# Optimization experiments

Hardware: AMD Instinct MI355X
Metric: run time of the kernel (lower is better)

Reference implementation:

```python
import jax, jax.numpy as jnp
import numpy as np

B, S, H, E, K = 4, 2048, 1024, 8, 2

def setup_inputs() -> dict:
    key = jax.random.key(0)
    k0, k1, k2, k3 = jax.random.split(key, 4)
    x = jax.random.normal(k0, (B, S, H), dtype=jnp.float32)
    # xavier-uniform-like scales
    router_w = jax.random.normal(k1, (E, H), dtype=jnp.float32) * np.float32(1.0 / np.sqrt(H))
    xav1 = np.float32(np.sqrt(2.0 / (2 * H + H)))
    w1 = jax.random.normal(k2, (E, 2 * H, H), dtype=jnp.float32) * xav1
    w2 = jax.random.normal(k3, (E, H, 2 * H), dtype=jnp.float32) * xav1
    return {"x": x, "router_w": router_w, "w1": w1, "w2": w2}

def reference(x, router_w, w1, w2):
    bsz, seq, hidden = x.shape
    n_experts = w1.shape[0]
    tokens = x.reshape(-1, hidden)                      # [T, H]
    T = tokens.shape[0]
    logits = tokens @ router_w.T                        # [T, E]
    topv, topi = jax.lax.top_k(logits, K)               # [T, K]
    w = jax.nn.softmax(topv, axis=-1).astype(tokens.dtype)
    # Dense gate matrix: gate[t, e] = routing weight of expert e for token t
    # (zero for non-selected experts). Equivalent to the torch pad/dispatch/
    # scatter-add combine: padded slots have weight 0 and contribute nothing.
    gate = jnp.zeros((T, n_experts), tokens.dtype).at[jnp.arange(T)[:, None], topi].add(w)
    out = jnp.zeros_like(tokens)
    for e in range(n_experts):  # small fixed expert count
        h = jax.nn.gelu(tokens @ w1[e].T, approximate=False)  # [T, 2H] (torch F.gelu = erf)
        y = h @ w2[e].T                                       # [T, H]
        out = out + gate[:, e:e + 1] * y
    return out.reshape(bsz, seq, hidden)
```

## Files before the change

### kernel.cpp

```cpp
#include <hip/hip_runtime.h>
#include <stdint.h>
#include <math.h>

#define T_TOK 8192
#define H_DIM 1024
#define H2    2048
#define NE    8

typedef unsigned short u16;
typedef __attribute__((ext_vector_type(8))) short bf16x8;
typedef __attribute__((ext_vector_type(4))) float f32x4;

__device__ __forceinline__ u16 f32_to_bf16(float f) {
  union { float f; unsigned u; } c; c.f = f;
  unsigned u = c.u + 0x7fffu + ((c.u >> 16) & 1u);
  return (u16)(u >> 16);
}
__device__ __forceinline__ float bf2f(u16 v) {
  union { unsigned u; float f; } c; c.u = (unsigned)v << 16; return c.f;
}

__device__ __forceinline__ float fast_gelu(float v) {
  float u = v * v;
  float z2 = v * fmaf(u, 0.1029437f, 2.3022078f);
  float e = __builtin_amdgcn_exp2f(z2);
  float r = __builtin_amdgcn_rcpf(1.0f + e);
  return v - v * r;
}

__device__ __forceinline__ void g2l16(const void* g, void* l) {
  __builtin_amdgcn_global_load_lds(
      (const __attribute__((address_space(1))) unsigned*)g,
      (__attribute__((address_space(3))) unsigned*)l, 16, 0, 0);
}

__device__ __forceinline__ int prefix_base(const int* counts, int e) {
  int b = 0;
#pragma unroll
  for (int j = 0; j < NE; j++) b += (j < e) ? counts[j] : 0;
  return b;
}

__global__ __launch_bounds__(256) void prep_kernel(
    const float* __restrict__ x, const float* __restrict__ rw,
    const float* __restrict__ w1, const float* __restrict__ w2,
    u16* __restrict__ xb, u16* __restrict__ w1b, u16* __restrict__ w2b,
    int* __restrict__ tope, float2* __restrict__ gate2,
    int* __restrict__ counts) {
  int blk = blockIdx.x;
  if (blk < T_TOK / 4) {
    int wave = threadIdx.x >> 6;
    int lane = threadIdx.x & 63;
    int t = blk * 4 + wave;
    const float4* x4 = (const float4*)(x + (size_t)t * H_DIM);
    const float4* rw4 = (const float4*)rw;
    u16* xbrow = xb + (size_t)t * H_DIM;

    double acc[NE];
#pragma unroll
    for (int e = 0; e < NE; e++) acc[e] = 0.0;
#pragma unroll
    for (int i = 0; i < 4; i++) {
      int c = lane + 64 * i;
      float4 xv = x4[c];
      ushort4 bv = make_ushort4(f32_to_bf16(xv.x), f32_to_bf16(xv.y),
                                f32_to_bf16(xv.z), f32_to_bf16(xv.w));
      *(ushort4*)(xbrow + c * 4) = bv;
#pragma unroll
      for (int e = 0; e < NE; e++) {
        float4 wv = rw4[e * 256 + c];
        acc[e] += (double)xv.x * wv.x + (double)xv.y * wv.y +
                  (double)xv.z * wv.z + (double)xv.w * wv.w;
      }
    }
#pragma unroll
    for (int off = 32; off >= 1; off >>= 1)
#pragma unroll
      for (int e = 0; e < NE; e++) acc[e] += __shfl_xor(acc[e], off, 64);

    if (lane == 0) {
      int e0 = 0; double v0 = acc[0];
#pragma unroll
      for (int e = 1; e < NE; e++) if (acc[e] > v0) { v0 = acc[e]; e0 = e; }
      int e1 = -1; double v1 = -1e300;
#pragma unroll
      for (int e = 0; e < NE; e++) if (e != e0 && acc[e] > v1) { v1 = acc[e]; e1 = e; }
      double ex = exp(v1 - v0);
      tope[t] = e0 | (e1 << 8);
      gate2[t] = make_float2((float)(1.0 / (1.0 + ex)), (float)(ex / (1.0 + ex)));
    }
  } else {
    int cb = blk - T_TOK / 4;
    if (cb == 0 && threadIdx.x < NE) counts[threadIdx.x] = 0;
    const float* src; u16* dst;
    if (cb < 3072) { src = w1; dst = w1b; }
    else           { src = w2; dst = w2b; cb -= 3072; }
    const int n4 = NE * H2 * H_DIM / 4;
    const int stride = 3072 * 256;
    const float4* s4 = (const float4*)src;
    for (int i = cb * 256 + threadIdx.x; i < n4; i += stride) {
      float4 v = s4[i];
      *(ushort4*)(dst + (size_t)i * 4) = make_ushort4(
          f32_to_bf16(v.x), f32_to_bf16(v.y), f32_to_bf16(v.z), f32_to_bf16(v.w));
    }
  }
}

__global__ __launch_bounds__(256) void build_kernel(
    const int* __restrict__ tope, int* __restrict__ counts,
    int* __restrict__ tok_list, int2* __restrict__ pos2) {
  __shared__ int cts[4][NE];
  __shared__ int gbase[NE];
  int tid = threadIdx.x, lane = tid & 63, w = tid >> 6;
  int t = blockIdx.x * 256 + tid;
  int pk = tope[t];
  int e0 = pk & 0xff, e1 = (pk >> 8) & 0xff;
  unsigned long long lt = ((unsigned long long)1 << lane) - 1;

  int r0 = 0, r1 = 0;
#pragma unroll
  for (int e = 0; e < NE; e++) {
    unsigned long long b0 = __ballot(e0 == e);
    unsigned long long b1 = __ballot(e1 == e);
    int n0 = __popcll(b0), n1 = __popcll(b1);
    if (e0 == e) r0 = __popcll(b0 & lt);
    if (e1 == e) r1 = n0 + __popcll(b1 & lt);
    if (lane == 0) cts[w][e] = n0 + n1;
  }
  __syncthreads();
  if (tid < NE) {
    int bt = cts[0][tid] + cts[1][tid] + cts[2][tid] + cts[3][tid];
    gbase[tid] = atomicAdd(&counts[tid], bt);
  }
  __syncthreads();
  int off0 = gbase[e0] + r0;
  int off1 = gbase[e1] + r1;
#pragma unroll
  for (int wp = 0; wp < 4; wp++) {
    if (wp < w) { off0 += cts[wp][e0]; off1 += cts[wp][e1]; }
  }
  tok_list[e0 * T_TOK + off0] = t;
  tok_list[e1 * T_TOK + off1] = t;
  pos2[t] = make_int2(off0, off1);
}

__global__ __launch_bounds__(256) void g1_kernel(
    const u16* __restrict__ xb, const u16* __restrict__ w1b,
    u16* __restrict__ h, const int* __restrict__ tok_list,
    const int* __restrict__ counts) {
  const int NT = H2 / 128;
  int e = blockIdx.x / (64 * NT);
  int rem = blockIdx.x % (64 * NT);
  int mt = rem / NT, nt = rem % NT;
  int cnt = counts[e];
  int m0 = mt * 128;
  if (m0 >= cnt) return;
  int base = prefix_base(counts, e);

  __shared__ u16 As[128 * 64];
  __shared__ u16 Bs[128 * 64];

  int tid = threadIdx.x;
  int lane = tid & 63, wave = tid >> 6;
  int wr = wave >> 1, wc = wave & 1;
  int quad = lane >> 4, l16 = lane & 15;
  int srow = tid >> 3;
  int cg = (tid & 7) ^ (srow & 7);

  const u16* w1e = w1b + (size_t)e * H2 * H_DIM;
  const u16* ap[4]; const u16* bp[4];
#pragma unroll
  for (int R = 0; R < 4; R++) {
    int r = m0 + R * 32 + srow; if (r > cnt - 1) r = cnt - 1;
    ap[R] = xb + (size_t)tok_list[e * T_TOK + r] * H_DIM + cg * 8;
    bp[R] = w1e + (size_t)(nt * 128 + R * 32 + srow) * H_DIM + cg * 8;
  }

  f32x4 acc[4][4];
#pragma unroll
  for (int i = 0; i < 4; i++)
#pragma unroll
    for (int j = 0; j < 4; j++)
#pragma unroll
      for (int r = 0; r < 4; r++) acc[i][j][r] = 0.f;

  int swz = l16 & 7;
  for (int k0 = 0; k0 < H_DIM; k0 += 64) {
#pragma unroll
    for (int R = 0; R < 4; R++) {
      g2l16(ap[R] + k0, As + R * 2048 + tid * 8);
      g2l16(bp[R] + k0, Bs + R * 2048 + tid * 8);
    }
    __syncthreads();
#pragma unroll
    for (int kk = 0; kk < 2; kk++) {
      bf16x8 af[4], bfr[4];
      int q = kk * 4 + quad;
#pragma unroll
      for (int mi = 0; mi < 4; mi++)
        af[mi] = *(const bf16x8*)(As + (wr * 64 + mi * 16 + l16) * 64 + ((q ^ swz) * 8));
#pragma unroll
      for (int ni = 0; ni < 4; ni++)
        bfr[ni] = *(const bf16x8*)(Bs + (wc * 64 + ni * 16 + l16) * 64 + ((q ^ swz) * 8));
#pragma unroll
      for (int mi = 0; mi < 4; mi++)
#pragma unroll
        for (int ni = 0; ni < 4; ni++)
          acc[mi][ni] = __builtin_amdgcn_mfma_f32_16x16x32_bf16(af[mi], bfr[ni], acc[mi][ni], 0, 0, 0);
    }
    __syncthreads();
  }

#pragma unroll
  for (int mi = 0; mi < 4; mi++) {
    int rbase = wr * 64 + mi * 16 + quad * 4;
#pragma unroll
    for (int r = 0; r < 4; r++) {
      int rr = m0 + rbase + r;
      if (rr < cnt) {
        size_t ho = (size_t)(base + rr) * H2 + nt * 128 + wc * 64 + l16;
#pragma unroll
        for (int ni = 0; ni < 4; ni++)
          h[ho + ni * 16] = f32_to_bf16(fast_gelu(acc[mi][ni][r]));
      }
    }
  }
}

__global__ __launch_bounds__(256) void g2_kernel(
    const u16* __restrict__ h, const u16* __restrict__ w2b,
    u16* __restrict__ y, const int* __restrict__ counts) {
  const int NT = H_DIM / 128;
  int e = blockIdx.x / (64 * NT);
  int rem = blockIdx.x % (64 * NT);
  int mt = rem / NT, nt = rem % NT;
  int cnt = counts[e];
  int m0 = mt * 128;
  if (m0 >= cnt) return;
  int base = prefix_base(counts, e);

  __shared__ u16 As[128 * 64];
  __shared__ u16 Bs[128 * 64];

  int tid = threadIdx.x;
  int lane = tid & 63, wave = tid >> 6;
  int wr = wave >> 1, wc = wave & 1;
  int quad = lane >> 4, l16 = lane & 15;
  int srow = tid >> 3;
  int cg = (tid & 7) ^ (srow & 7);

  const u16* w2e = w2b + (size_t)e * H_DIM * H2;
  const u16* ap[4]; const u16* bp[4];
#pragma unroll
  for (int R = 0; R < 4; R++) {
    int r = m0 + R * 32 + srow; if (r > cnt - 1) r = cnt - 1;
    ap[R] = h + (size_t)(base + r) * H2 + cg * 8;
    bp[R] = w2e + (size_t)(nt * 128 + R * 32 + srow) * H2 + cg * 8;
  }

  f32x4 acc[4][4];
#pragma unroll
  for (int i = 0; i < 4; i++)
#pragma unroll
    for (int j = 0; j < 4; j++)
#pragma unroll
      for (int r = 0; r < 4; r++) acc[i][j][r] = 0.f;

  int swz = l16 & 7;
  for (int k0 = 0; k0 < H2; k0 += 64) {
#pragma unroll
    for (int R = 0; R < 4; R++) {
      g2l16(ap[R] + k0, As + R * 2048 + tid * 8);
      g2l16(bp[R] + k0, Bs + R * 2048 + tid * 8);
    }
    __syncthreads();
#pragma unroll
    for (int kk = 0; kk < 2; kk++) {
      bf16x8 af[4], bfr[4];
      int q = kk * 4 + quad;
#pragma unroll
      for (int mi = 0; mi < 4; mi++)
        af[mi] = *(const bf16x8*)(As + (wr * 64 + mi * 16 + l16) * 64 + ((q ^ swz) * 8));
#pragma unroll
      for (int ni = 0; ni < 4; ni++)
        bfr[ni] = *(const bf16x8*)(Bs + (wc * 64 + ni * 16 + l16) * 64 + ((q ^ swz) * 8));
#pragma unroll
      for (int mi = 0; mi < 4; mi++)
#pragma unroll
        for (int ni = 0; ni < 4; ni++)
          acc[mi][ni] = __builtin_amdgcn_mfma_f32_16x16x32_bf16(af[mi], bfr[ni], acc[mi][ni], 0, 0, 0);
    }
    __syncthreads();
  }

#pragma unroll
  for (int mi = 0; mi < 4; mi++) {
    int rbase = wr * 64 + mi * 16 + quad * 4;
#pragma unroll
    for (int r = 0; r < 4; r++) {
      int rr = m0 + rbase + r;
      if (rr < cnt) {
        size_t yo = (size_t)(base + rr) * H_DIM + nt * 128 + wc * 64 + l16;
#pragma unroll
        for (int ni = 0; ni < 4; ni++)
          y[yo + ni * 16] = f32_to_bf16(acc[mi][ni][r]);
      }
    }
  }
}

__global__ __launch_bounds__(256) void combine_kernel(
    const u16* __restrict__ y, const int* __restrict__ tope,
    const float2* __restrict__ gate2, const int2* __restrict__ pos2,
    const int* __restrict__ counts, float* __restrict__ out) {
  int t = blockIdx.x;
  int pk = tope[t];
  int e0 = pk & 0xff, e1 = (pk >> 8) & 0xff;
  float2 g = gate2[t];
  int2 p = pos2[t];
  int hb0 = prefix_base(counts, e0);
  int hb1 = prefix_base(counts, e1);
  size_t s0 = (size_t)(hb0 + p.x) * H_DIM + threadIdx.x * 4;
  size_t s1 = (size_t)(hb1 + p.y) * H_DIM + threadIdx.x * 4;
  ushort4 a = *(const ushort4*)(y + s0);
  ushort4 b = *(const ushort4*)(y + s1);
  float4 o;
  o.x = g.x * bf2f(a.x) + g.y * bf2f(b.x);
  o.y = g.x * bf2f(a.y) + g.y * bf2f(b.y);
  o.z = g.x * bf2f(a.z) + g.y * bf2f(b.z);
  o.w = g.x * bf2f(a.w) + g.y * bf2f(b.w);
  *(float4*)(out + (size_t)t * H_DIM + threadIdx.x * 4) = o;
}

extern "C" void kernel_launch(void* const* d_in, const int* in_sizes, int n_in,
                              void* d_out, int out_size, void* d_ws, size_t ws_size,
                              hipStream_t stream) {
  const float* x  = (const float*)d_in[0];
  const float* rw = (const float*)d_in[1];
  const float* w1 = (const float*)d_in[2];
  const float* w2 = (const float*)d_in[3];
  float* out = (float*)d_out;

  char* ws = (char*)d_ws;
  u16* xb       = (u16*)(ws);
  u16* w1b      = (u16*)(ws + 16777216);
  u16* y        = (u16*)(ws + 16777216);
  u16* w2b      = (u16*)(ws + 50331648);
  u16* h        = (u16*)(ws + 83886080);
  int* tok_list = (int*)(ws + 150994944);
  int* tope     = (int*)(ws + 151257088);
  float2* gate2 = (float2*)(ws + 151289856);
  int2* pos2    = (int2*)(ws + 151355392);
  int* counts   = (int*)(ws + 151420928);

  prep_kernel<<<T_TOK / 4 + 6144, 256, 0, stream>>>(x, rw, w1, w2, xb, w1b, w2b,
                                                    tope, gate2, counts);
  build_kernel<<<T_TOK / 256, 256, 0, stream>>>(tope, counts, tok_list, pos2);
  g1_kernel<<<NE * 64 * (H2 / 128), 256, 0, stream>>>(xb, w1b, h, tok_list, counts);
  g2_kernel<<<NE * 64 * (H_DIM / 128), 256, 0, stream>>>(h, w2b, y, counts);
  combine_kernel<<<T_TOK, 256, 0, stream>>>(y, tope, gate2, pos2, counts, out);
}
```

Measured before the change: 406.8 us.

## Unify expert GEMMs into pipelined 256x256 tile kernel with 4-stage LDS ring

Replaces the two separate 128x128 expert GEMM kernels with one templated kernel that uses 256x256 output tiles, 512 threads (8 waves, 2x4), and a K-step of 32. Global-to-LDS loads go through a 4-deep buffer ring with explicit vmcnt waits, so loads for step k+3 are in flight while step k runs its MFMAs. The change also adds s_setprio around the MFMA block and drops the second barrier per iteration. The goal is to hide global memory latency and raise data reuse per tile. The cost is higher register pressure (128 accumulators per thread) and 128KB of LDS per block, and larger tiles waste more work on partial per-expert tiles.

New measurement: 400.8 us. Within noise of the previous version (-1.5%).

```diff
diff --git a/kernel.cpp b/kernel.cpp
--- a/kernel.cpp
+++ b/kernel.cpp
@@ -144,166 +144,112 @@
   pos2[t] = make_int2(off0, off1);
 }
 
-__global__ __launch_bounds__(256) void g1_kernel(
-    const u16* __restrict__ xb, const u16* __restrict__ w1b,
-    u16* __restrict__ h, const int* __restrict__ tok_list,
+template <int NK, int NT, int OUTN, bool GATHER, bool GELU>
+__global__ __launch_bounds__(512, 2) void moe_gemm(
+    const u16* __restrict__ A, const u16* __restrict__ W,
+    u16* __restrict__ O, const int* __restrict__ tok_list,
     const int* __restrict__ counts) {
-  const int NT = H2 / 128;
-  int e = blockIdx.x / (64 * NT);
-  int rem = blockIdx.x % (64 * NT);
+  const int MTMAX = T_TOK / 256;
+  int e = blockIdx.x / (MTMAX * NT);
+  int rem = blockIdx.x % (MTMAX * NT);
   int mt = rem / NT, nt = rem % NT;
   int cnt = counts[e];
-  int m0 = mt * 128;
+  int m0 = mt * 256;
   if (m0 >= cnt) return;
   int base = prefix_base(counts, e);
-
-  __shared__ u16 As[128 * 64];
-  __shared__ u16 Bs[128 * 64];
+  const int K = NK * 32;
+
+  __shared__ u16 lA[4][8192];
+  __shared__ u16 lB[4][8192];
 
   int tid = threadIdx.x;
   int lane = tid & 63, wave = tid >> 6;
-  int wr = wave >> 1, wc = wave & 1;
+  int wr = wave >> 2, wc = wave & 3;
   int quad = lane >> 4, l16 = lane & 15;
-  int srow = tid >> 3;
-  int cg = (tid & 7) ^ (srow & 7);
-
-  const u16* w1e = w1b + (size_t)e * H2 * H_DIM;
-  const u16* ap[4]; const u16* bp[4];
-#pragma unroll
-  for (int R = 0; R < 4; R++) {
-    int r = m0 + R * 32 + srow; if (r > cnt - 1) r = cnt - 1;
-    ap[R] = xb + (size_t)tok_list[e * T_TOK + r] * H_DIM + cg * 8;
-    bp[R] = w1e + (size_t)(nt * 128 + R * 32 + srow) * H_DIM + cg * 8;
-  }
-
-  f32x4 acc[4][4];
-#pragma unroll
-  for (int i = 0; i < 4; i++)
+
+  int cg = (tid & 3) ^ ((tid >> 3) & 3);
+  const u16* We = W + (size_t)e * OUTN * K;
+  const u16* asrc[2]; const u16* bsrc[2];
+#pragma unroll
+  for (int r = 0; r < 2; ++r) {
+    int row = (tid >> 2) + 128 * r;
+    int ar = m0 + row; if (ar > cnt - 1) ar = cnt - 1;
+    if (GATHER) asrc[r] = A + (size_t)tok_list[e * T_TOK + ar] * K + cg * 8;
+    else        asrc[r] = A + (size_t)(base + ar) * K + cg * 8;
+    bsrc[r] = We + (size_t)(nt * 256 + row) * K + cg * 8;
+  }
+
+  auto stage = [&](int kt) {
+    int b = kt & 3;
+#pragma unroll
+    for (int r = 0; r < 2; ++r) {
+      g2l16(asrc[r] + kt * 32, &lA[b][r * 4096 + tid * 8]);
+      g2l16(bsrc[r] + kt * 32, &lB[b][r * 4096 + tid * 8]);
+    }
+  };
+
+  f32x4 acc[8][4];
+#pragma unroll
+  for (int i = 0; i < 8; i++)
 #pragma unroll
     for (int j = 0; j < 4; j++)
 #pragma unroll
       for (int r = 0; r < 4; r++) acc[i][j][r] = 0.f;
 
-  int swz = l16 & 7;
-  for (int k0 = 0; k0 < H_DIM; k0 += 64) {
-#pragma unroll
-    for (int R = 0; R < 4; R++) {
-      g2l16(ap[R] + k0, As + R * 2048 + tid * 8);
-      g2l16(bp[R] + k0, Bs + R * 2048 + tid * 8);
-    }
-    __syncthreads();
-#pragma unroll
-    for (int kk = 0; kk < 2; kk++) {
-      bf16x8 af[4], bfr[4];
-      int q = kk * 4 + quad;
-#pragma unroll
-      for (int mi = 0; mi < 4; mi++)
-        af[mi] = *(const bf16x8*)(As + (wr * 64 + mi * 16 + l16) * 64 + ((q ^ swz) * 8));
-#pragma unroll
-      for (int ni = 0; ni < 4; ni++)
-        bfr[ni] = *(const bf16x8*)(Bs + (wc * 64 + ni * 16 + l16) * 64 + ((q ^ swz) * 8));
-#pragma unroll
-      for (int mi = 0; mi < 4; mi++)
-#pragma unroll
-        for (int ni = 0; ni < 4; ni++)
-          acc[mi][ni] = __builtin_amdgcn_mfma_f32_16x16x32_bf16(af[mi], bfr[ni], acc[mi][ni], 0, 0, 0);
-    }
-    __syncthreads();
-  }
-
-#pragma unroll
-  for (int mi = 0; mi < 4; mi++) {
-    int rbase = wr * 64 + mi * 16 + quad * 4;
-#pragma unroll
-    for (int r = 0; r < 4; r++) {
-      int rr = m0 + rbase + r;
-      if (rr < cnt) {
-        size_t ho = (size_t)(base + rr) * H2 + nt * 128 + wc * 64 + l16;
-#pragma unroll
-        for (int ni = 0; ni < 4; ni++)
-          h[ho + ni * 16] = f32_to_bf16(fast_gelu(acc[mi][ni][r]));
-      }
-    }
-  }
-}
-
-__global__ __launch_bounds__(256) void g2_kernel(
-    const u16* __restrict__ h, const u16* __restrict__ w2b,
-    u16* __restrict__ y, const int* __restrict__ counts) {
-  const int NT = H_DIM / 128;
-  int e = blockIdx.x / (64 * NT);
-  int rem = blockIdx.x % (64 * NT);
-  int mt = rem / NT, nt = rem % NT;
-  int cnt = counts[e];
-  int m0 = mt * 128;
-  if (m0 >= cnt) return;
-  int base = prefix_base(counts, e);
-
-  __shared__ u16 As[128 * 64];
-  __shared__ u16 Bs[128 * 64];
-
-  int tid = threadIdx.x;
-  int lane = tid & 63, wave = tid >> 6;
-  int wr = wave >> 1, wc = wave & 1;
-  int quad = lane >> 4, l16 = lane & 15;
-  int srow = tid >> 3;
-  int cg = (tid & 7) ^ (srow & 7);
-
-  const u16* w2e = w2b + (size_t)e * H_DIM * H2;
-  const u16* ap[4]; const u16* bp[4];
-#pragma unroll
-  for (int R = 0; R < 4; R++) {
-    int r = m0 + R * 32 + srow; if (r > cnt - 1) r = cnt - 1;
-    ap[R] = h + (size_t)(base + r) * H2 + cg * 8;
-    bp[R] = w2e + (size_t)(nt * 128 + R * 32 + srow) * H2 + cg * 8;
-  }
-
-  f32x4 acc[4][4];
-#pragma unroll
-  for (int i = 0; i < 4; i++)
-#pragma unroll
-    for (int j = 0; j < 4; j++)
-#pragma unroll
-      for (int r = 0; r < 4; r++) acc[i][j][r] = 0.f;
-
-  int swz = l16 & 7;
-  for (int k0 = 0; k0 < H2; k0 += 64) {
-#pragma unroll
-    for (int R = 0; R < 4; R++) {
-      g2l16(ap[R] + k0, As + R * 2048 + tid * 8);
-      g2l16(bp[R] + k0, Bs + R * 2048 + tid * 8);
-    }
-    __syncthreads();
-#pragma unroll
-    for (int kk = 0; kk < 2; kk++) {
-      bf16x8 af[4], bfr[4];
-      int q = kk * 4 + quad;
-#pragma unroll
-      for (int mi = 0; mi < 4; mi++)
-        af[mi] = *(const bf16x8*)(As + (wr * 64 + mi * 16 + l16) * 64 + ((q ^ swz) * 8));
-#pragma unroll
-      for (int ni = 0; ni < 4; ni++)
-        bfr[ni] = *(const bf16x8*)(Bs + (wc * 64 + ni * 16 + l16) * 64 + ((q ^ swz) * 8));
-#pragma unroll
-      for (int mi = 0; mi < 4; mi++)
-#pragma unroll
-        for (int ni = 0; ni < 4; ni++)
-          acc[mi][ni] = __builtin_amdgcn_mfma_f32_16x16x32_bf16(af[mi], bfr[ni], acc[mi][ni], 0, 0, 0);
-    }
-    __syncthreads();
-  }
-
-#pragma unroll
-  for (int mi = 0; mi < 4; mi++) {
-    int rbase = wr * 64 + mi * 16 + quad * 4;
-#pragma unroll
-    for (int r = 0; r < 4; r++) {
-      int rr = m0 + rbase + r;
-      if (rr < cnt) {
-        size_t yo = (size_t)(base + rr) * H_DIM + nt * 128 + wc * 64 + l16;
-#pragma unroll
-        for (int ni = 0; ni < 4; ni++)
-          y[yo + ni * 16] = f32_to_bf16(acc[mi][ni][r]);
+  stage(0); stage(1); stage(2);
+  asm volatile("s_waitcnt vmcnt(8)" ::: "memory");
+  __builtin_amdgcn_s_barrier();
+  __builtin_amdgcn_sched_barrier(0);
+
+  int aoff = (wr * 128 + l16) * 32 + (quad ^ ((l16 >> 1) & 3)) * 8;
+  int boff = (wc * 64 + l16) * 32 + (quad ^ ((l16 >> 1) & 3)) * 8;
+
+#pragma unroll 1
+  for (int k = 0; k < NK; ++k) {
+    const u16* Ab = &lA[k & 3][0] + aoff;
+    const u16* Bb = &lB[k & 3][0] + boff;
+    bf16x8 af[8], bfr[4];
+#pragma unroll
+    for (int mi = 0; mi < 8; ++mi)
+      af[mi] = *(const bf16x8*)(Ab + mi * 512);
+#pragma unroll
+    for (int ni = 0; ni < 4; ++ni)
+      bfr[ni] = *(const bf16x8*)(Bb + ni * 512);
+
+    if (k + 3 < NK) stage(k + 3);
+
+    __builtin_amdgcn_s_setprio(1);
+#pragma unroll
+    for (int mi = 0; mi < 8; ++mi)
+#pragma unroll
+      for (int ni = 0; ni < 4; ++ni)
+        acc[mi][ni] = __builtin_amdgcn_mfma_f32_16x16x32_bf16(
+            af[mi], bfr[ni], acc[mi][ni], 0, 0, 0);
+    __builtin_amdgcn_s_setprio(0);
+
+    if (k + 3 < NK)      asm volatile("s_waitcnt vmcnt(8)" ::: "memory");
+    else if (k + 2 < NK) asm volatile("s_waitcnt vmcnt(4)" ::: "memory");
+    else if (k + 1 < NK) asm volatile("s_waitcnt vmcnt(0)" ::: "memory");
+    if (k + 1 < NK) {
+      __builtin_amdgcn_s_barrier();
+      __builtin_amdgcn_sched_barrier(0);
+    }
+  }
+
+#pragma unroll
+  for (int mi = 0; mi < 8; ++mi) {
+    int rb = wr * 128 + mi * 16 + quad * 4;
+#pragma unroll
+    for (int r = 0; r < 4; ++r) {
+      int grow = m0 + rb + r;
+      if (grow < cnt) {
+        size_t o = (size_t)(base + grow) * OUTN + nt * 256 + wc * 64 + l16;
+#pragma unroll
+        for (int ni = 0; ni < 4; ++ni) {
+          float v = acc[mi][ni][r];
+          if (GELU) v = fast_gelu(v);
+          O[o + ni * 16] = f32_to_bf16(v);
+        }
       }
     }
   }
@@ -356,7 +302,9 @@
   prep_kernel<<<T_TOK / 4 + 6144, 256, 0, stream>>>(x, rw, w1, w2, xb, w1b, w2b,
                                                     tope, gate2, counts);
   build_kernel<<<T_TOK / 256, 256, 0, stream>>>(tope, counts, tok_list, pos2);
-  g1_kernel<<<NE * 64 * (H2 / 128), 256, 0, stream>>>(xb, w1b, h, tok_list, counts);
-  g2_kernel<<<NE * 64 * (H_DIM / 128), 256, 0, stream>>>(h, w2b, y, counts);
+  moe_gemm<32, 8, H2, true, true>
+      <<<NE * 32 * 8, 512, 0, stream>>>(xb, w1b, h, tok_list, counts);
+  moe_gemm<64, 4, H_DIM, false, false>
+      <<<NE * 32 * 4, 512, 0, stream>>>(h, w2b, y, tok_list, counts);
   combine_kernel<<<T_TOK, 256, 0, stream>>>(y, tope, gate2, pos2, counts, out);
 }
```
